# Kernel optimization log

Measured on AMD Instinct MI355X. Metric: run time of the kernel, lower is better.

Reference implementation:

```python
import jax, jax.numpy as jnp
import numpy as np

H = 8  # heads hardcoded in LightGFormer


def layernorm(x, g, b, eps=1e-5):
    m = x.mean(-1, keepdims=True)
    v = ((x - m) ** 2).mean(-1, keepdims=True)
    return (x - m) / jnp.sqrt(v + eps) * g + b


def setup_inputs() -> dict:
    key = jax.random.key(0)
    B, N, D, L = 16, 512, 256, 4
    Dff = 4 * D
    ks = jax.random.split(key, 12)

    def w(k, shape, scale=0.02):
        return jax.random.normal(k, shape, jnp.float32) * scale

    return {
        "input": w(ks[0], (B, N, D), 1.0),
        "input_v": w(ks[1], (B, N, D), 1.0),
        "pos_emb": w(ks[2], (N, D)),
        "Wq": w(ks[3], (L, D, D)), "bq": jnp.zeros((L, D), jnp.float32),
        "Wk": w(ks[4], (L, D, D)), "bk": jnp.zeros((L, D), jnp.float32),
        "Wv": w(ks[5], (L, D, D)), "bv": jnp.zeros((L, D), jnp.float32),
        "Wo": w(ks[6], (L, D, D)), "bo": jnp.zeros((L, D), jnp.float32),
        "W1": w(ks[7], (L, D, Dff)), "b1": jnp.zeros((L, Dff), jnp.float32),
        "W2": w(ks[8], (L, Dff // 2, D // 2)), "b2": jnp.zeros((L, D // 2), jnp.float32),
        "g1": jnp.ones((L, D), jnp.float32), "be1": jnp.zeros((L, D), jnp.float32),
        "g2": jnp.ones((L, D), jnp.float32), "be2": jnp.zeros((L, D), jnp.float32),
        "gf": jnp.ones((D,), jnp.float32), "bf": jnp.zeros((D,), jnp.float32),
        "mask": jax.random.randint(ks[9], (N, N), 0, 2) > 0,
    }


def reference(input, input_v, pos_emb, Wq, bq, Wk, bk, Wv, bv, Wo, bo,
              W1, b1, W2, b2, g1, be1, g2, be2, gf, bf, mask):
    B, N, D = input.shape
    L = Wq.shape[0]
    dk = D // H
    scale = 1.0 / float(np.sqrt(dk))

    x = input + pos_emb[None]       # learned positional encoding
    xv = input_v + pos_emb[None]    # values stream (never updated across layers)

    for i in range(L):
        # --- self-attention: queries/keys from x, values from xv ---
        q = (x @ Wq[i] + bq[i]).reshape(B, N, H, dk)
        k = (x @ Wk[i] + bk[i]).reshape(B, N, H, dk)
        v = (xv @ Wv[i] + bv[i]).reshape(B, N, H, dk)
        att = jnp.einsum('bqhd,bkhd->bhqk', q, k) * scale
        if i % 2 == 1:  # odd layers use the mask (Lightformer alternation)
            att = jnp.where(mask[None, None], -jnp.inf, att)
        att = jax.nn.softmax(att, axis=-1)
        o = jnp.einsum('bhqk,bkhd->bqhd', att, v).reshape(B, N, D)
        o = o @ Wo[i] + bo[i]
        x = layernorm(x + o, g1[i], be1[i])
        # --- FFN with grouped second linear: [.., 2, 2D] @ [2D, D/2] ---
        h = jax.nn.gelu(x @ W1[i] + b1[i], approximate=False)
        h = (h.reshape(B, N, 2, 2 * D) @ W2[i] + b2[i]).reshape(B, N, D)
        x = layernorm(x + h, g2[i], be2[i])

    x = layernorm(x, gf, bf)  # final attention_norm
    return x
```

## Files before the change

kernel.cpp:

```cpp
#include <hip/hip_runtime.h>
#include <hip/hip_bf16.h>
#include <math.h>

#define BDIM 16
#define NSEQ 512
#define DMODEL 256
#define NLAYER 4
#define NHEAD 8
#define DK 32
#define DFF 1024
#define BN (BDIM * NSEQ)
#define ND (NSEQ * DMODEL)

typedef __bf16 bf16x8 __attribute__((ext_vector_type(8)));
typedef float floatx4 __attribute__((ext_vector_type(4)));
typedef unsigned uint32x2 __attribute__((ext_vector_type(2)));

static __device__ __forceinline__ unsigned short f2bf(float f) {
    unsigned u = __float_as_uint(f);
    unsigned r = (u + 0x7FFFu + ((u >> 16) & 1u)) >> 16;
    return (unsigned short)r;
}

static __device__ __forceinline__ void async_ld16(const unsigned short* g,
                                                  unsigned short* l) {
    __builtin_amdgcn_global_load_lds(
        (const __attribute__((address_space(1))) unsigned int*)g,
        (__attribute__((address_space(3))) unsigned int*)l, 16, 0, 0);
}

static __device__ __forceinline__ float gelu_f(float c) {
    float u = 0.7978845608028654f * (c + 0.044715f * c * c * c);
    return c * (1.f / (1.f + __expf(-2.f * u)));
}

__global__ void conv_all_kernel(const float* __restrict__ Wq, const float* __restrict__ Wk,
                                const float* __restrict__ Wv, const float* __restrict__ Wo,
                                const float* __restrict__ W1, const float* __restrict__ W2,
                                const int* __restrict__ mask,
                                unsigned short* __restrict__ wqT, unsigned short* __restrict__ wkT,
                                unsigned short* __restrict__ wvT, unsigned short* __restrict__ woT,
                                unsigned short* __restrict__ w1T, unsigned short* __restrict__ w2T,
                                unsigned* __restrict__ bits) {
    int blk = blockIdx.x, tid = threadIdx.x;
    if (blk < 4096) {
        int i = blk * 256 + tid;
        int sel = i >> 18;
        int j = i & 262143;
        int l = j >> 16, rem = j & 65535, kk = rem >> 8, n = rem & 255;
        const float* src = sel == 0 ? Wq : sel == 1 ? Wk : sel == 2 ? Wv : Wo;
        unsigned short* dst = sel == 0 ? wqT : sel == 1 ? wkT : sel == 2 ? wvT : woT;
        dst[(size_t)l * 65536 + n * 256 + kk] = f2bf(src[j]);
    } else if (blk < 8192) {
        int i = (blk - 4096) * 256 + tid;
        int l = i >> 18, rem = i & 262143, kk = rem >> 10, n = rem & 1023;
        w1T[(size_t)l * 262144 + (size_t)n * 256 + kk] = f2bf(W1[i]);
    } else if (blk < 9216) {
        int j = (blk - 8192) * 256 + tid;
        int l = j >> 16, rem = j & 65535, kk = rem >> 7, n = rem & 127;
        w2T[(size_t)l * 65536 + (size_t)n * 512 + kk] = f2bf(W2[j]);
    } else {
        int w = (blk - 9216) * 256 + tid;
        int r = w >> 4, wi = w & 15;
        const int* src = mask + r * NSEQ + wi * 32;
        unsigned acc = 0;
#pragma unroll
        for (int j = 0; j < 32; j++) acc |= (src[j] != 0 ? 1u : 0u) << j;
        bits[w] = acc;
    }
}

__global__ void add_pos_kernel(const float* __restrict__ in,
                               const float* __restrict__ inv,
                               const float* __restrict__ pos,
                               float* __restrict__ x,
                               unsigned short* __restrict__ xb,
                               unsigned short* __restrict__ xvb,
                               int total) {
    int i = blockIdx.x * blockDim.x + threadIdx.x;
    if (i < total) {
        float pe = pos[i % ND];
        float a = in[i] + pe;
        float b = inv[i] + pe;
        x[i] = a;
        xb[i] = f2bf(a);
        xvb[i] = f2bf(b);
    }
}

__global__ __launch_bounds__(256) void qkv_mfma_kernel(
        const unsigned short* __restrict__ xb,
        const unsigned short* __restrict__ xvb,
        const unsigned short* __restrict__ WqT, const unsigned short* __restrict__ WkT,
        const unsigned short* __restrict__ WvT,
        const float* __restrict__ bq, const float* __restrict__ bk,
        const float* __restrict__ bv,
        unsigned short* __restrict__ qo, unsigned short* __restrict__ ko,
        unsigned short* __restrict__ vo) {
    int proj = blockIdx.x >> 1;
    const unsigned short* A  = (proj == 2) ? xvb : xb;
    const unsigned short* Bt = (proj == 0) ? WqT : (proj == 1) ? WkT : WvT;
    const float* bias        = (proj == 0) ? bq  : (proj == 1) ? bk  : bv;
    unsigned short* Cb       = (proj == 0) ? qo  : (proj == 1) ? ko  : vo;
    float qscale = (proj == 0) ? 0.17677669529663687f : 1.f;

    __shared__ unsigned short As[128 * 32];
    __shared__ unsigned short Bs[128 * 32];
    int tid = threadIdx.x;
    int wave = tid >> 6, lane = tid & 63;
    int rowBase = blockIdx.y * 128, colBase = (blockIdx.x & 1) * 128;
    int m0w = (wave & 1) * 64, n0w = (wave >> 1) * 64;
    int lr = lane & 15, quad = lane >> 4;
    int qx = quad ^ (lr & 3);

    floatx4 acc[4][4];
#pragma unroll
    for (int mi = 0; mi < 4; mi++)
#pragma unroll
        for (int nj = 0; nj < 4; nj++) acc[mi][nj] = (floatx4)0.0f;

    for (int kt = 0; kt < DMODEL; kt += 32) {
#pragma unroll
        for (int t = 0; t < 2; t++) {
            int idx = t * 256 + tid;
            int row = idx >> 2, kv8 = ((idx ^ row) & 3) * 8;
            async_ld16(A + (size_t)(rowBase + row) * DMODEL + kt + kv8, &As[idx * 8]);
            async_ld16(Bt + (size_t)(colBase + row) * DMODEL + kt + kv8, &Bs[idx * 8]);
        }
        __syncthreads();
        bf16x8 af[4], bfr[4];
#pragma unroll
        for (int mi = 0; mi < 4; mi++)
            af[mi] = *(const bf16x8*)&As[(m0w + mi * 16 + lr) * 32 + qx * 8];
#pragma unroll
        for (int nj = 0; nj < 4; nj++)
            bfr[nj] = *(const bf16x8*)&Bs[(n0w + nj * 16 + lr) * 32 + qx * 8];
#pragma unroll
        for (int mi = 0; mi < 4; mi++)
#pragma unroll
            for (int nj = 0; nj < 4; nj++)
                acc[mi][nj] = __builtin_amdgcn_mfma_f32_16x16x32_bf16(
                    af[mi], bfr[nj], acc[mi][nj], 0, 0, 0);
        __syncthreads();
    }

#pragma unroll
    for (int mi = 0; mi < 4; mi++) {
#pragma unroll
        for (int r = 0; r < 4; r++) {
            int grow = rowBase + m0w + mi * 16 + quad * 4 + r;
#pragma unroll
            for (int nj = 0; nj < 4; nj++) {
                int gcol = colBase + n0w + nj * 16 + lr;
                float c = (acc[mi][nj][r] + bias[gcol]) * qscale;
                size_t off = ((size_t)((grow >> 9) * 8 + (gcol >> 5)) << 14)
                           + (size_t)(grow & 511) * 32 + (gcol & 31);
                Cb[off] = f2bf(c);
            }
        }
    }
}

__global__ __launch_bounds__(256) void gemm_mfma_kernel(
        const unsigned short* __restrict__ A,
        const unsigned short* __restrict__ Bt,
        const float* __restrict__ bias,
        unsigned short* __restrict__ Cb,
        int M, int K, int N, int act) {
    __shared__ unsigned short As[128 * 32];
    __shared__ unsigned short Bs[128 * 32];
    int tid = threadIdx.x;
    int wave = tid >> 6, lane = tid & 63;
    int rowBase = blockIdx.y * 128, colBase = blockIdx.x * 128;
    int m0w = (wave & 1) * 64, n0w = (wave >> 1) * 64;
    int lr = lane & 15, quad = lane >> 4;
    int qx = quad ^ (lr & 3);

    floatx4 acc[4][4];
#pragma unroll
    for (int mi = 0; mi < 4; mi++)
#pragma unroll
        for (int nj = 0; nj < 4; nj++) acc[mi][nj] = (floatx4)0.0f;

    for (int kt = 0; kt < K; kt += 32) {
#pragma unroll
        for (int t = 0; t < 2; t++) {
            int idx = t * 256 + tid;
            int row = idx >> 2, kv8 = ((idx ^ row) & 3) * 8;
            async_ld16(A + (size_t)(rowBase + row) * K + kt + kv8, &As[idx * 8]);
            async_ld16(Bt + (size_t)(colBase + row) * K + kt + kv8, &Bs[idx * 8]);
        }
        __syncthreads();
        bf16x8 af[4], bfr[4];
#pragma unroll
        for (int mi = 0; mi < 4; mi++)
            af[mi] = *(const bf16x8*)&As[(m0w + mi * 16 + lr) * 32 + qx * 8];
#pragma unroll
        for (int nj = 0; nj < 4; nj++)
            bfr[nj] = *(const bf16x8*)&Bs[(n0w + nj * 16 + lr) * 32 + qx * 8];
#pragma unroll
        for (int mi = 0; mi < 4; mi++)
#pragma unroll
            for (int nj = 0; nj < 4; nj++)
                acc[mi][nj] = __builtin_amdgcn_mfma_f32_16x16x32_bf16(
                    af[mi], bfr[nj], acc[mi][nj], 0, 0, 0);
        __syncthreads();
    }

#pragma unroll
    for (int mi = 0; mi < 4; mi++) {
#pragma unroll
        for (int r = 0; r < 4; r++) {
            int grow = rowBase + m0w + mi * 16 + quad * 4 + r;
#pragma unroll
            for (int nj = 0; nj < 4; nj++) {
                int gcol = colBase + n0w + nj * 16 + lr;
                float c = acc[mi][nj][r] + bias[gcol];
                if (act) c = gelu_f(c);
                Cb[(size_t)grow * N + gcol] = f2bf(c);
            }
        }
    }
}

__global__ __launch_bounds__(64) void wo_ln_kernel(
        const unsigned short* __restrict__ A,
        const unsigned short* __restrict__ Bt,
        const float* __restrict__ bias,
        const float* __restrict__ g, const float* __restrict__ be,
        float* __restrict__ xf, unsigned short* __restrict__ xb) {
    __shared__ unsigned short As[16 * 32];
    __shared__ unsigned short Bs[256 * 32];
    int tid = threadIdx.x;
    int l16 = tid & 15, quad = tid >> 4;
    int rowBase = blockIdx.x * 16;
    int qx = quad ^ (l16 & 3);

    floatx4 acc[16];
#pragma unroll
    for (int t = 0; t < 16; t++) acc[t] = (floatx4)0.0f;

    for (int kt = 0; kt < 256; kt += 32) {
        {
            int row = tid >> 2, kv8 = ((tid ^ row) & 3) * 8;
            async_ld16(A + (size_t)(rowBase + row) * 256 + kt + kv8, &As[tid * 8]);
        }
#pragma unroll
        for (int t = 0; t < 16; t++) {
            int idx = t * 64 + tid;
            int row = idx >> 2, kv8 = ((idx ^ row) & 3) * 8;
            async_ld16(Bt + (size_t)row * 256 + kt + kv8, &Bs[idx * 8]);
        }
        __syncthreads();
        bf16x8 af = *(const bf16x8*)&As[l16 * 32 + qx * 8];
#pragma unroll
        for (int t = 0; t < 16; t++) {
            bf16x8 bfr = *(const bf16x8*)&Bs[(t * 16 + l16) * 32 + qx * 8];
            acc[t] = __builtin_amdgcn_mfma_f32_16x16x32_bf16(af, bfr, acc[t], 0, 0, 0);
        }
        __syncthreads();
    }

    float bcol[16], gc[16], bec[16];
#pragma unroll
    for (int t = 0; t < 16; t++) {
        int c = t * 16 + l16;
        bcol[t] = bias[c]; gc[t] = g[c]; bec[t] = be[c];
    }
#pragma unroll
    for (int r = 0; r < 4; r++) {
        int grow = rowBase + quad * 4 + r;
        float v[16], s = 0.f, s2 = 0.f;
#pragma unroll
        for (int t = 0; t < 16; t++) {
            int c = t * 16 + l16;
            float val = acc[t][r] + bcol[t] + xf[(size_t)grow * 256 + c];
            v[t] = val; s += val; s2 += val * val;
        }
#pragma unroll
        for (int off = 1; off <= 8; off <<= 1) {
            s += __shfl_xor(s, off);
            s2 += __shfl_xor(s2, off);
        }
        float mean = s * (1.f / 256.f);
        float var = s2 * (1.f / 256.f) - mean * mean;
        float rstd = rsqrtf(var + 1e-5f);
#pragma unroll
        for (int t = 0; t < 16; t++) {
            int c = t * 16 + l16;
            float o = (v[t] - mean) * rstd * gc[t] + bec[t];
            xf[(size_t)grow * 256 + c] = o;
            xb[(size_t)grow * 256 + c] = f2bf(o);
        }
    }
}

__global__ __launch_bounds__(128) void ffn2_ln_kernel(
        const unsigned short* __restrict__ A,
        const unsigned short* __restrict__ Bt,
        const float* __restrict__ bias,
        const float* __restrict__ g, const float* __restrict__ be,
        float* __restrict__ xf, unsigned short* __restrict__ xb) {
    __shared__ unsigned short As[64 * 32];
    __shared__ unsigned short Bs[128 * 32];
    __shared__ float redS[64][2], redQ[64][2];
    int tid = threadIdx.x;
    int wave = tid >> 6, lane = tid & 63, l16 = lane & 15, quad = lane >> 4;
    int rowBase = blockIdx.x * 64;
    int n0w = wave * 64;
    int qx = quad ^ (l16 & 3);

    floatx4 acc[4][4];
#pragma unroll
    for (int mi = 0; mi < 4; mi++)
#pragma unroll
        for (int nj = 0; nj < 4; nj++) acc[mi][nj] = (floatx4)0.0f;

    for (int kt = 0; kt < 512; kt += 32) {
#pragma unroll
        for (int t = 0; t < 2; t++) {
            int idx = t * 128 + tid;
            int row = idx >> 2, kv8 = ((idx ^ row) & 3) * 8;
            async_ld16(A + (size_t)(rowBase + row) * 512 + kt + kv8, &As[idx * 8]);
        }
#pragma unroll
        for (int t = 0; t < 4; t++) {
            int idx = t * 128 + tid;
            int row = idx >> 2, kv8 = ((idx ^ row) & 3) * 8;
            async_ld16(Bt + (size_t)row * 512 + kt + kv8, &Bs[idx * 8]);
        }
        __syncthreads();
        bf16x8 af[4], bfr[4];
#pragma unroll
        for (int mi = 0; mi < 4; mi++)
            af[mi] = *(const bf16x8*)&As[(mi * 16 + l16) * 32 + qx * 8];
#pragma unroll
        for (int nj = 0; nj < 4; nj++)
            bfr[nj] = *(const bf16x8*)&Bs[(n0w + nj * 16 + l16) * 32 + qx * 8];
#pragma unroll
        for (int mi = 0; mi < 4; mi++)
#pragma unroll
            for (int nj = 0; nj < 4; nj++)
                acc[mi][nj] = __builtin_amdgcn_mfma_f32_16x16x32_bf16(
                    af[mi], bfr[nj], acc[mi][nj], 0, 0, 0);
        __syncthreads();
    }

#pragma unroll
    for (int mi = 0; mi < 4; mi++) {
#pragma unroll
        for (int r = 0; r < 4; r++) {
            int row = mi * 16 + quad * 4 + r;
            int grow = rowBase + row;
            int token = grow >> 1, dbase = (grow & 1) * 128;
            float s = 0.f, s2 = 0.f;
#pragma unroll
            for (int nj = 0; nj < 4; nj++) {
                int gcol = n0w + nj * 16 + l16;
                float val = acc[mi][nj][r] + bias[gcol]
                          + xf[(size_t)token * 256 + dbase + gcol];
                acc[mi][nj][r] = val;
                s += val; s2 += val * val;
            }
#pragma unroll
            for (int off = 1; off <= 8; off <<= 1) {
                s += __shfl_xor(s, off);
                s2 += __shfl_xor(s2, off);
            }
            if (l16 == 0) { redS[row][wave] = s; redQ[row][wave] = s2; }
        }
    }
    __syncthreads();

#pragma unroll
    for (int mi = 0; mi < 4; mi++) {
#pragma unroll
        for (int r = 0; r < 4; r++) {
            int row = mi * 16 + quad * 4 + r;
            int grow = rowBase + row;
            int token = grow >> 1, dbase = (grow & 1) * 128;
            float ts = redS[row][0] + redS[row][1] + redS[row ^ 1][0] + redS[row ^ 1][1];
            float tq = redQ[row][0] + redQ[row][1] + redQ[row ^ 1][0] + redQ[row ^ 1][1];
            float mean = ts * (1.f / 256.f);
            float var = tq * (1.f / 256.f) - mean * mean;
            float rstd = rsqrtf(var + 1e-5f);
#pragma unroll
            for (int nj = 0; nj < 4; nj++) {
                int gcol = n0w + nj * 16 + l16;
                int d = dbase + gcol;
                float o = (acc[mi][nj][r] - mean) * rstd * g[d] + be[d];
                xf[(size_t)token * 256 + d] = o;
                xb[(size_t)token * 256 + d] = f2bf(o);
            }
        }
    }
}

__global__ __launch_bounds__(256, 4) void attn_mfma_kernel(
        const unsigned short* __restrict__ q, const unsigned short* __restrict__ k,
        const unsigned short* __restrict__ v, unsigned short* __restrict__ o,
        const unsigned* __restrict__ mbits_g, int use_mask) {
    int bid = blockIdx.x;
    int qg = bid >> 7;
    int bh = bid & 127;
    int h = bh & 7, b = bh >> 3;
    int tid = threadIdx.x;

    __shared__ unsigned short Vs[2][NSEQ * 16];

    const unsigned short* kbase = k + (size_t)(b * 8 + h) * (NSEQ * DK);
    const unsigned short* vbase = v + (size_t)(b * 8 + h) * (NSEQ * DK);

#pragma unroll
    for (int db = 0; db < 2; db++) {
#pragma unroll
        for (int t = 0; t < 4; t++) {
            int c = t * 256 + tid;
            int kk = c >> 1, half = c & 1;
            async_ld16(vbase + (size_t)kk * 32 + db * 16 + half * 8,
                       &Vs[db][c * 8]);
        }
    }

    int wave = tid >> 6, lane = tid & 63, l16 = lane & 15, quad = lane >> 4;
    int qbase = qg * 64 + wave * 16;

    bf16x8 qf = *(const bf16x8*)(q + ((size_t)(b * 8 + h) * NSEQ + qbase + l16) * 32 + quad * 8);

    unsigned mw[16];
    if (use_mask) {
        const uint4* mr = (const uint4*)(mbits_g + (size_t)(qbase + l16) * 16);
#pragma unroll
        for (int w = 0; w < 4; w++) *(uint4*)&mw[w * 4] = mr[w];
    } else {
#pragma unroll
        for (int w = 0; w < 16; w++) mw[w] = 0;
    }
    __syncthreads();

    unsigned va0 = (unsigned)(size_t)&Vs[0][0] + (unsigned)(lane * 8);
    unsigned va1 = (unsigned)(size_t)&Vs[1][0] + (unsigned)(lane * 8);

    const unsigned short* kfrag = kbase + (size_t)l16 * DK + quad * 8;

    floatx4 oT0 = (floatx4)0.f, oT1 = (floatx4)0.f;
    float m_run = -INFINITY, l_part = 0.f;

    uint32x2 t00, t01, t10, t11;
#define TR_ISSUE(cc)                                                      \
    asm volatile("ds_read_b64_tr_b16 %0, %4\n\t"                          \
                 "ds_read_b64_tr_b16 %1, %4 offset:512\n\t"               \
                 "ds_read_b64_tr_b16 %2, %5\n\t"                          \
                 "ds_read_b64_tr_b16 %3, %5 offset:512"                   \
                 : "=&v"(t00), "=&v"(t01), "=&v"(t10), "=&v"(t11)         \
                 : "v"(va0 + (unsigned)((cc) * 1024)),                    \
                   "v"(va1 + (unsigned)((cc) * 1024)))
    TR_ISSUE(0);

    bf16x8 k0 = *(const bf16x8*)(kfrag);
    bf16x8 k1 = *(const bf16x8*)(kfrag + 16 * DK);

#pragma unroll
    for (int c = 0; c < 16; c++) {
        floatx4 s0 = __builtin_amdgcn_mfma_f32_16x16x32_bf16(k0, qf, (floatx4)0.f, 0, 0, 0);
        floatx4 s1 = __builtin_amdgcn_mfma_f32_16x16x32_bf16(k1, qf, (floatx4)0.f, 0, 0, 0);

        bf16x8 k0n, k1n;
        if (c < 15) {
            k0n = *(const bf16x8*)(kfrag + (size_t)((c + 1) * 32) * DK);
            k1n = *(const bf16x8*)(kfrag + (size_t)((c + 1) * 32 + 16) * DK);
        }

        float sv[8];
#pragma unroll
        for (int r = 0; r < 4; r++) { sv[r] = s0[r]; sv[4 + r] = s1[r]; }
        if (use_mask) {
            unsigned wb = mw[c];
#pragma unroll
            for (int r = 0; r < 4; r++) {
                if ((wb >> (quad * 4 + r)) & 1) sv[r] = -INFINITY;
                if ((wb >> (16 + quad * 4 + r)) & 1) sv[4 + r] = -INFINITY;
            }
        }
        float mx = fmaxf(fmaxf(fmaxf(sv[0], sv[1]), fmaxf(sv[2], sv[3])),
                         fmaxf(fmaxf(sv[4], sv[5]), fmaxf(sv[6], sv[7])));
        mx = fmaxf(mx, __shfl_xor(mx, 16));
        mx = fmaxf(mx, __shfl_xor(mx, 32));
        if (!__all(mx <= m_run)) {
            float mnew = fmaxf(m_run, mx);
            float corr = (m_run == mnew) ? 1.f : __expf(m_run - mnew);
            l_part *= corr;
            oT0 *= corr; oT1 *= corr;
            m_run = mnew;
        }
        float p[8];
#pragma unroll
        for (int j = 0; j < 8; j++) {
            float e = __expf(sv[j] - m_run);
            p[j] = (sv[j] > -INFINITY) ? e : 0.f;
            l_part += p[j];
        }
        union { bf16x8 v8; unsigned u[4]; } pf;
#pragma unroll
        for (int j = 0; j < 4; j++)
            asm("v_cvt_pk_bf16_f32 %0, %1, %2"
                : "=v"(pf.u[j]) : "v"(p[2 * j]), "v"(p[2 * j + 1]));

        asm volatile("s_waitcnt lgkmcnt(0)");
        __builtin_amdgcn_sched_barrier(0);
        union { bf16x8 v8; uint32x2 u[2]; } av0, av1;
        av0.u[0] = t00; av0.u[1] = t01;
        av1.u[0] = t10; av1.u[1] = t11;

        oT0 = __builtin_amdgcn_mfma_f32_16x16x32_bf16(av0.v8, pf.v8, oT0, 0, 0, 0);
        oT1 = __builtin_amdgcn_mfma_f32_16x16x32_bf16(av1.v8, pf.v8, oT1, 0, 0, 0);
        if (c < 15) TR_ISSUE(c + 1);
        k0 = k0n; k1 = k1n;
    }
#undef TR_ISSUE

    float l = l_part;
    l += __shfl_xor(l, 16);
    l += __shfl_xor(l, 32);
    float invl = (l > 0.f) ? 1.f / l : 0.f;

    unsigned short* orow = o + ((size_t)(b * NSEQ + qbase + l16)) * DMODEL + h * DK;
#pragma unroll
    for (int r = 0; r < 4; r++) {
        orow[quad * 4 + r]      = f2bf(oT0[r] * invl);
        orow[16 + quad * 4 + r] = f2bf(oT1[r] * invl);
    }
}

__global__ __launch_bounds__(256) void final_ln_kernel(
        const float* __restrict__ a,
        const float* __restrict__ g, const float* __restrict__ be,
        float* __restrict__ out) {
    int t = blockIdx.x;
    int d = threadIdx.x;
    size_t idx = (size_t)t * DMODEL + d;
    float v = a[idx];
    float s = v, s2 = v * v;
#pragma unroll
    for (int off = 32; off; off >>= 1) {
        s  += __shfl_xor(s, off);
        s2 += __shfl_xor(s2, off);
    }
    __shared__ float ws1[4], ws2[4];
    int wid = d >> 6;
    if ((d & 63) == 0) { ws1[wid] = s; ws2[wid] = s2; }
    __syncthreads();
    s  = ws1[0] + ws1[1] + ws1[2] + ws1[3];
    s2 = ws2[0] + ws2[1] + ws2[2] + ws2[3];
    float mean = s * (1.f / DMODEL);
    float var = s2 * (1.f / DMODEL) - mean * mean;
    float rstd = rsqrtf(var + 1e-5f);
    out[idx] = (v - mean) * rstd * g[d] + be[d];
}

extern "C" void kernel_launch(void* const* d_in, const int* in_sizes, int n_in,
                              void* d_out, int out_size, void* d_ws, size_t ws_size,
                              hipStream_t stream) {
    const float* input  = (const float*)d_in[0];
    const float* inputv = (const float*)d_in[1];
    const float* pos    = (const float*)d_in[2];
    const float* Wq = (const float*)d_in[3];
    const float* bq = (const float*)d_in[4];
    const float* Wk = (const float*)d_in[5];
    const float* bk = (const float*)d_in[6];
    const float* Wv = (const float*)d_in[7];
    const float* bv = (const float*)d_in[8];
    const float* Wo = (const float*)d_in[9];
    const float* bo = (const float*)d_in[10];
    const float* W1 = (const float*)d_in[11];
    const float* b1 = (const float*)d_in[12];
    const float* W2 = (const float*)d_in[13];
    const float* b2 = (const float*)d_in[14];
    const float* g1 = (const float*)d_in[15];
    const float* be1 = (const float*)d_in[16];
    const float* g2 = (const float*)d_in[17];
    const float* be2 = (const float*)d_in[18];
    const float* gf = (const float*)d_in[19];
    const float* bff = (const float*)d_in[20];
    const int* mask = (const int*)d_in[21];

    float* out = (float*)d_out;

    char* wsb = (char*)d_ws;
    float* x_f  = (float*)(wsb + ((size_t)0 << 20));
    unsigned short* x_b  = (unsigned short*)(wsb + ((size_t)8 << 20));
    unsigned short* xv_b = (unsigned short*)(wsb + ((size_t)12 << 20));
    unsigned short* qb_b = (unsigned short*)(wsb + ((size_t)16 << 20));
    unsigned short* kb_b = (unsigned short*)(wsb + ((size_t)20 << 20));
    unsigned short* vb_b = (unsigned short*)(wsb + ((size_t)24 << 20));
    unsigned short* ab_b = (unsigned short*)(wsb + ((size_t)28 << 20));
    unsigned short* h_b  = qb_b;
    unsigned short* wqT = (unsigned short*)(wsb + ((size_t)32 << 20));
    unsigned short* wkT = wqT + (size_t)4 * 65536;
    unsigned short* wvT = wkT + (size_t)4 * 65536;
    unsigned short* woT = wvT + (size_t)4 * 65536;
    unsigned short* w1T = woT + (size_t)4 * 65536;
    unsigned short* w2T = w1T + (size_t)4 * 262144;
    unsigned* mbits = (unsigned*)(wsb + ((size_t)37 << 20));

    const size_t TOK = (size_t)BN * DMODEL;

    conv_all_kernel<<<9248, 256, 0, stream>>>(Wq, Wk, Wv, Wo, W1, W2, mask,
                                              wqT, wkT, wvT, woT, w1T, w2T, mbits);
    add_pos_kernel<<<(int)((TOK + 255) / 256), 256, 0, stream>>>(
        input, inputv, pos, x_f, x_b, xv_b, (int)TOK);

    for (int i = 0; i < NLAYER; i++) {
        const unsigned short* WqT_i = wqT + (size_t)i * 65536;
        const unsigned short* WkT_i = wkT + (size_t)i * 65536;
        const unsigned short* WvT_i = wvT + (size_t)i * 65536;
        const unsigned short* WoT_i = woT + (size_t)i * 65536;
        const unsigned short* W1T_i = w1T + (size_t)i * 262144;
        const unsigned short* W2T_i = w2T + (size_t)i * 65536;

        qkv_mfma_kernel<<<dim3(6, 64), 256, 0, stream>>>(
            x_b, xv_b, WqT_i, WkT_i, WvT_i,
            bq + i * DMODEL, bk + i * DMODEL, bv + i * DMODEL,
            qb_b, kb_b, vb_b);

        attn_mfma_kernel<<<BDIM * NHEAD * 8, 256, 0, stream>>>(
            qb_b, kb_b, vb_b, ab_b, mbits, (i & 1));

        wo_ln_kernel<<<BN / 16, 64, 0, stream>>>(
            ab_b, WoT_i, bo + i * DMODEL,
            g1 + i * DMODEL, be1 + i * DMODEL, x_f, x_b);

        gemm_mfma_kernel<<<dim3(8, 64), 256, 0, stream>>>(
            x_b, W1T_i, b1 + i * DFF, h_b, BN, DMODEL, DFF, 1);

        ffn2_ln_kernel<<<(2 * BN) / 64, 128, 0, stream>>>(
            h_b, W2T_i, b2 + i * (DMODEL / 2),
            g2 + i * DMODEL, be2 + i * DMODEL, x_f, x_b);
    }

    final_ln_kernel<<<BN, DMODEL, 0, stream>>>(x_f, gf, bff, out);
}
```

Before: 454.6 us.

## Fuse Wo+LN1, FFN1+GELU, FFN2+LN2 and final LN into one kernel per layer

Replaces the separate Wo+LayerNorm, W1 GEMM with GELU, W2+LayerNorm and final LayerNorm kernels with one fused per-16-token kernel. The intermediate activations (post-LN1 x and the GELU hidden) stay in LDS and are read with transposed LDS reads. Weights are pre-swizzled into MFMA fragment order so they can be loaded straight from global memory, and attention writes its output in fragment-panel layout. This removes the round trip of the large FFN hidden tensor through global memory and several launches. In exchange, each 16-row block re-reads every layer weight from global or cache, and parallelism per block is small.

```diff
diff --git a/kernel.cpp b/kernel.cpp
--- a/kernel.cpp
+++ b/kernel.cpp
@@ -21,6 +21,9 @@
     unsigned r = (u + 0x7FFFu + ((u >> 16) & 1u)) >> 16;
     return (unsigned short)r;
 }
+static __device__ __forceinline__ float bf2f(unsigned short u) {
+    return __uint_as_float(((unsigned)u) << 16);
+}
 
 static __device__ __forceinline__ void async_ld16(const unsigned short* g,
                                                   unsigned short* l) {
@@ -34,31 +37,54 @@
     return c * (1.f / (1.f + __expf(-2.f * u)));
 }
 
+static __device__ __forceinline__ unsigned cvtpk(float lo, float hi) {
+    unsigned r;
+    asm("v_cvt_pk_bf16_f32 %0, %1, %2" : "=v"(r) : "v"(lo), "v"(hi));
+    return r;
+}
+
 __global__ void conv_all_kernel(const float* __restrict__ Wq, const float* __restrict__ Wk,
                                 const float* __restrict__ Wv, const float* __restrict__ Wo,
                                 const float* __restrict__ W1, const float* __restrict__ W2,
                                 const int* __restrict__ mask,
                                 unsigned short* __restrict__ wqT, unsigned short* __restrict__ wkT,
-                                unsigned short* __restrict__ wvT, unsigned short* __restrict__ woT,
-                                unsigned short* __restrict__ w1T, unsigned short* __restrict__ w2T,
+                                unsigned short* __restrict__ wvT,
+                                unsigned short* __restrict__ wo_s,
+                                unsigned short* __restrict__ w1_s, unsigned short* __restrict__ w2_s,
                                 unsigned* __restrict__ bits) {
     int blk = blockIdx.x, tid = threadIdx.x;
-    if (blk < 4096) {
+    if (blk < 3072) {
         int i = blk * 256 + tid;
         int sel = i >> 18;
         int j = i & 262143;
         int l = j >> 16, rem = j & 65535, kk = rem >> 8, n = rem & 255;
-        const float* src = sel == 0 ? Wq : sel == 1 ? Wk : sel == 2 ? Wv : Wo;
-        unsigned short* dst = sel == 0 ? wqT : sel == 1 ? wkT : sel == 2 ? wvT : woT;
+        const float* src = sel == 0 ? Wq : sel == 1 ? Wk : Wv;
+        unsigned short* dst = sel == 0 ? wqT : sel == 1 ? wkT : wvT;
         dst[(size_t)l * 65536 + n * 256 + kk] = f2bf(src[j]);
+    } else if (blk < 4096) {
+        int i = (blk - 3072) * 256 + tid;
+        int l = i >> 16, o = i & 65535;
+        int j = o & 7, quad = (o >> 3) & 3, l16 = (o >> 5) & 15;
+        int kt = (o >> 9) & 7, cg = (o >> 12) & 15;
+        int k = kt * 32 + (j >> 2) * 16 + quad * 4 + (j & 3);
+        int dout = cg * 16 + l16;
+        wo_s[(size_t)l * 65536 + o] = f2bf(Wo[(size_t)l * 65536 + k * 256 + dout]);
     } else if (blk < 8192) {
         int i = (blk - 4096) * 256 + tid;
-        int l = i >> 18, rem = i & 262143, kk = rem >> 10, n = rem & 1023;
-        w1T[(size_t)l * 262144 + (size_t)n * 256 + kk] = f2bf(W1[i]);
+        int l = i >> 18, o = i & 262143;
+        int j = o & 7, quad = (o >> 3) & 3, l16 = (o >> 5) & 15;
+        int kt = (o >> 9) & 7, cg = (o >> 12) & 63;
+        int k = kt * 32 + (j >> 2) * 16 + quad * 4 + (j & 3);
+        int dout = cg * 16 + l16;
+        w1_s[(size_t)l * 262144 + o] = f2bf(W1[(size_t)l * 262144 + k * 1024 + dout]);
     } else if (blk < 9216) {
-        int j = (blk - 8192) * 256 + tid;
-        int l = j >> 16, rem = j & 65535, kk = rem >> 7, n = rem & 127;
-        w2T[(size_t)l * 65536 + (size_t)n * 512 + kk] = f2bf(W2[j]);
+        int i = (blk - 8192) * 256 + tid;
+        int l = i >> 16, o = i & 65535;
+        int j = o & 7, quad = (o >> 3) & 3, l16 = (o >> 5) & 15;
+        int kt = (o >> 9) & 15, cg = (o >> 13) & 7;
+        int k = kt * 32 + (j >> 2) * 16 + quad * 4 + (j & 3);
+        int dout = cg * 16 + l16;
+        w2_s[(size_t)l * 65536 + o] = f2bf(W2[(size_t)l * 65536 + k * 128 + dout]);
     } else {
         int w = (blk - 9216) * 256 + tid;
         int r = w >> 4, wi = w & 15;
@@ -161,244 +187,257 @@
     }
 }
 
-__global__ __launch_bounds__(256) void gemm_mfma_kernel(
-        const unsigned short* __restrict__ A,
-        const unsigned short* __restrict__ Bt,
-        const float* __restrict__ bias,
-        unsigned short* __restrict__ Cb,
-        int M, int K, int N, int act) {
-    __shared__ unsigned short As[128 * 32];
-    __shared__ unsigned short Bs[128 * 32];
+__global__ __launch_bounds__(256) void ffn_fused_kernel(
+        const unsigned short* __restrict__ ab_f,
+        const unsigned short* __restrict__ wo_s,
+        const unsigned short* __restrict__ w1_s,
+        const unsigned short* __restrict__ w2_s,
+        const float* __restrict__ bo,
+        const float* __restrict__ g1, const float* __restrict__ be1,
+        const float* __restrict__ b1,
+        const float* __restrict__ b2,
+        const float* __restrict__ g2, const float* __restrict__ be2,
+        const float* __restrict__ gf, const float* __restrict__ bf_,
+        float* __restrict__ xf, unsigned short* __restrict__ xb,
+        float* __restrict__ outF, int finalize) {
+    __shared__ unsigned short X1s[8 * 512];
+    __shared__ unsigned short Hs[16 * 512];
+    __shared__ float redA[16][4], redB[16][4];
+    __shared__ float redC[16][4], redD[16][4];
+    __shared__ float redE[16][4], redF[16][4];
+
     int tid = threadIdx.x;
-    int wave = tid >> 6, lane = tid & 63;
-    int rowBase = blockIdx.y * 128, colBase = blockIdx.x * 128;
-    int m0w = (wave & 1) * 64, n0w = (wave >> 1) * 64;
-    int lr = lane & 15, quad = lane >> 4;
-    int qx = quad ^ (lr & 3);
-
-    floatx4 acc[4][4];
-#pragma unroll
-    for (int mi = 0; mi < 4; mi++)
-#pragma unroll
-        for (int nj = 0; nj < 4; nj++) acc[mi][nj] = (floatx4)0.0f;
-
-    for (int kt = 0; kt < K; kt += 32) {
-#pragma unroll
-        for (int t = 0; t < 2; t++) {
-            int idx = t * 256 + tid;
-            int row = idx >> 2, kv8 = ((idx ^ row) & 3) * 8;
-            async_ld16(A + (size_t)(rowBase + row) * K + kt + kv8, &As[idx * 8]);
-            async_ld16(Bt + (size_t)(colBase + row) * K + kt + kv8, &Bs[idx * 8]);
-        }
-        __syncthreads();
-        bf16x8 af[4], bfr[4];
-#pragma unroll
-        for (int mi = 0; mi < 4; mi++)
-            af[mi] = *(const bf16x8*)&As[(m0w + mi * 16 + lr) * 32 + qx * 8];
-#pragma unroll
-        for (int nj = 0; nj < 4; nj++)
-            bfr[nj] = *(const bf16x8*)&Bs[(n0w + nj * 16 + lr) * 32 + qx * 8];
-#pragma unroll
-        for (int mi = 0; mi < 4; mi++)
-#pragma unroll
-            for (int nj = 0; nj < 4; nj++)
-                acc[mi][nj] = __builtin_amdgcn_mfma_f32_16x16x32_bf16(
-                    af[mi], bfr[nj], acc[mi][nj], 0, 0, 0);
-        __syncthreads();
-    }
-
-#pragma unroll
-    for (int mi = 0; mi < 4; mi++) {
-#pragma unroll
-        for (int r = 0; r < 4; r++) {
-            int grow = rowBase + m0w + mi * 16 + quad * 4 + r;
-#pragma unroll
-            for (int nj = 0; nj < 4; nj++) {
-                int gcol = colBase + n0w + nj * 16 + lr;
-                float c = acc[mi][nj][r] + bias[gcol];
-                if (act) c = gelu_f(c);
-                Cb[(size_t)grow * N + gcol] = f2bf(c);
-            }
-        }
-    }
-}
-
-__global__ __launch_bounds__(64) void wo_ln_kernel(
-        const unsigned short* __restrict__ A,
-        const unsigned short* __restrict__ Bt,
-        const float* __restrict__ bias,
-        const float* __restrict__ g, const float* __restrict__ be,
-        float* __restrict__ xf, unsigned short* __restrict__ xb) {
-    __shared__ unsigned short As[16 * 32];
-    __shared__ unsigned short Bs[256 * 32];
-    int tid = threadIdx.x;
-    int l16 = tid & 15, quad = tid >> 4;
-    int rowBase = blockIdx.x * 16;
-    int qx = quad ^ (l16 & 3);
-
-    floatx4 acc[16];
-#pragma unroll
-    for (int t = 0; t < 16; t++) acc[t] = (floatx4)0.0f;
-
-    for (int kt = 0; kt < 256; kt += 32) {
-        {
-            int row = tid >> 2, kv8 = ((tid ^ row) & 3) * 8;
-            async_ld16(A + (size_t)(rowBase + row) * 256 + kt + kv8, &As[tid * 8]);
-        }
-#pragma unroll
-        for (int t = 0; t < 16; t++) {
-            int idx = t * 64 + tid;
-            int row = idx >> 2, kv8 = ((idx ^ row) & 3) * 8;
-            async_ld16(Bt + (size_t)row * 256 + kt + kv8, &Bs[idx * 8]);
-        }
-        __syncthreads();
-        bf16x8 af = *(const bf16x8*)&As[l16 * 32 + qx * 8];
-#pragma unroll
-        for (int t = 0; t < 16; t++) {
-            bf16x8 bfr = *(const bf16x8*)&Bs[(t * 16 + l16) * 32 + qx * 8];
-            acc[t] = __builtin_amdgcn_mfma_f32_16x16x32_bf16(af, bfr, acc[t], 0, 0, 0);
-        }
-        __syncthreads();
-    }
-
-    float bcol[16], gc[16], bec[16];
-#pragma unroll
-    for (int t = 0; t < 16; t++) {
-        int c = t * 16 + l16;
-        bcol[t] = bias[c]; gc[t] = g[c]; bec[t] = be[c];
-    }
+    int w = tid >> 6, lane = tid & 63, l16 = lane & 15, quad = lane >> 4;
+    int bid = blockIdx.x;
+    int rowBase = bid * 16;
+    int fo = (l16 * 4 + quad) * 8;
+
+#define TR2(d0, d1, addr)                                                  \
+    asm volatile("ds_read_b64_tr_b16 %0, %2\n\t"                           \
+                 "ds_read_b64_tr_b16 %1, %2 offset:512"                    \
+                 : "=&v"(d0), "=&v"(d1) : "v"(addr))
+
+    floatx4 accA[4];
+#pragma unroll
+    for (int cg = 0; cg < 4; cg++) accA[cg] = (floatx4)0.0f;
+
+#pragma unroll
+    for (int kt = 0; kt < 8; kt++) {
+        bf16x8 af = *(const bf16x8*)(ab_f + ((size_t)bid * 8 + kt) * 512 + fo);
+        bf16x8 bfr[4];
+#pragma unroll
+        for (int cg = 0; cg < 4; cg++)
+            bfr[cg] = *(const bf16x8*)(wo_s + ((size_t)((w * 4 + cg) * 8 + kt)) * 512 + fo);
+#pragma unroll
+        for (int cg = 0; cg < 4; cg++)
+            accA[cg] = __builtin_amdgcn_mfma_f32_16x16x32_bf16(af, bfr[cg], accA[cg], 0, 0, 0);
+    }
+
 #pragma unroll
     for (int r = 0; r < 4; r++) {
-        int grow = rowBase + quad * 4 + r;
-        float v[16], s = 0.f, s2 = 0.f;
-#pragma unroll
-        for (int t = 0; t < 16; t++) {
-            int c = t * 16 + l16;
-            float val = acc[t][r] + bcol[t] + xf[(size_t)grow * 256 + c];
-            v[t] = val; s += val; s2 += val * val;
+        int tok = quad * 4 + r;
+        float s = 0.f, s2 = 0.f;
+#pragma unroll
+        for (int cg = 0; cg < 4; cg++) {
+            int col = w * 64 + cg * 16 + l16;
+            float v = accA[cg][r] + bo[col] + xf[(size_t)(rowBase + tok) * 256 + col];
+            accA[cg][r] = v; s += v; s2 += v * v;
         }
 #pragma unroll
         for (int off = 1; off <= 8; off <<= 1) {
             s += __shfl_xor(s, off);
             s2 += __shfl_xor(s2, off);
         }
-        float mean = s * (1.f / 256.f);
-        float var = s2 * (1.f / 256.f) - mean * mean;
+        if (l16 == 0) { redA[tok][w] = s; redB[tok][w] = s2; }
+    }
+    __syncthreads();
+#pragma unroll
+    for (int r = 0; r < 4; r++) {
+        int tok = quad * 4 + r;
+        float ts = redA[tok][0] + redA[tok][1] + redA[tok][2] + redA[tok][3];
+        float tq = redB[tok][0] + redB[tok][1] + redB[tok][2] + redB[tok][3];
+        float mean = ts * (1.f / 256.f);
+        float var = tq * (1.f / 256.f) - mean * mean;
         float rstd = rsqrtf(var + 1e-5f);
 #pragma unroll
-        for (int t = 0; t < 16; t++) {
-            int c = t * 16 + l16;
-            float o = (v[t] - mean) * rstd * gc[t] + bec[t];
-            xf[(size_t)grow * 256 + c] = o;
-            xb[(size_t)grow * 256 + c] = f2bf(o);
-        }
-    }
-}
-
-__global__ __launch_bounds__(128) void ffn2_ln_kernel(
-        const unsigned short* __restrict__ A,
-        const unsigned short* __restrict__ Bt,
-        const float* __restrict__ bias,
-        const float* __restrict__ g, const float* __restrict__ be,
-        float* __restrict__ xf, unsigned short* __restrict__ xb) {
-    __shared__ unsigned short As[64 * 32];
-    __shared__ unsigned short Bs[128 * 32];
-    __shared__ float redS[64][2], redQ[64][2];
-    int tid = threadIdx.x;
-    int wave = tid >> 6, lane = tid & 63, l16 = lane & 15, quad = lane >> 4;
-    int rowBase = blockIdx.x * 64;
-    int n0w = wave * 64;
-    int qx = quad ^ (l16 & 3);
-
-    floatx4 acc[4][4];
-#pragma unroll
-    for (int mi = 0; mi < 4; mi++)
-#pragma unroll
-        for (int nj = 0; nj < 4; nj++) acc[mi][nj] = (floatx4)0.0f;
-
-    for (int kt = 0; kt < 512; kt += 32) {
-#pragma unroll
-        for (int t = 0; t < 2; t++) {
-            int idx = t * 128 + tid;
-            int row = idx >> 2, kv8 = ((idx ^ row) & 3) * 8;
-            async_ld16(A + (size_t)(rowBase + row) * 512 + kt + kv8, &As[idx * 8]);
-        }
-#pragma unroll
-        for (int t = 0; t < 4; t++) {
-            int idx = t * 128 + tid;
-            int row = idx >> 2, kv8 = ((idx ^ row) & 3) * 8;
-            async_ld16(Bt + (size_t)row * 512 + kt + kv8, &Bs[idx * 8]);
+        for (int cg = 0; cg < 4; cg++) {
+            int col = w * 64 + cg * 16 + l16;
+            accA[cg][r] = (accA[cg][r] - mean) * rstd * g1[col] + be1[col];
+        }
+    }
+#pragma unroll
+    for (int cg = 0; cg < 4; cg++) {
+        int col = w * 64 + cg * 16 + l16;
+        int ct = col >> 5, colL = col & 31;
+        uint32x2 pk;
+        pk[0] = cvtpk(accA[cg][0], accA[cg][1]);
+        pk[1] = cvtpk(accA[cg][2], accA[cg][3]);
+        *(uint32x2*)&X1s[ct * 512 + colL * 16 + quad * 4] = pk;
+    }
+    __syncthreads();
+
+    unsigned x1addr = (unsigned)(size_t)&X1s[0] + (unsigned)(lane * 8);
+    unsigned haddr  = (unsigned)(size_t)&Hs[0]  + (unsigned)(lane * 8);
+
+    floatx4 y[2][2];
+#pragma unroll
+    for (int g = 0; g < 2; g++)
+#pragma unroll
+        for (int cj = 0; cj < 2; cj++) y[g][cj] = (floatx4)0.0f;
+
+    for (int g = 0; g < 2; g++) {
+        floatx4 accB[8];
+#pragma unroll
+        for (int c = 0; c < 8; c++) accB[c] = (floatx4)0.0f;
+
+        uint32x2 ta, tb;
+        TR2(ta, tb, x1addr);
+#pragma unroll
+        for (int kt = 0; kt < 8; kt++) {
+            bf16x8 bfr[8];
+#pragma unroll
+            for (int c = 0; c < 8; c++)
+                bfr[c] = *(const bf16x8*)(w1_s +
+                    ((size_t)((g * 32 + w * 8 + c) * 8 + kt)) * 512 + fo);
+            asm volatile("s_waitcnt lgkmcnt(0)");
+            __builtin_amdgcn_sched_barrier(0);
+            union { bf16x8 v8; uint32x2 u[2]; } afu;
+            afu.u[0] = ta; afu.u[1] = tb;
+            bf16x8 af = afu.v8;
+            if (kt < 7) TR2(ta, tb, x1addr + (unsigned)((kt + 1) * 1024));
+#pragma unroll
+            for (int c = 0; c < 8; c++)
+                accB[c] = __builtin_amdgcn_mfma_f32_16x16x32_bf16(af, bfr[c], accB[c], 0, 0, 0);
+        }
+#pragma unroll
+        for (int c = 0; c < 8; c++) {
+            int col = w * 128 + c * 16 + l16;
+            float bb = b1[g * 512 + col];
+            float o0 = gelu_f(accB[c][0] + bb);
+            float o1 = gelu_f(accB[c][1] + bb);
+            float o2 = gelu_f(accB[c][2] + bb);
+            float o3 = gelu_f(accB[c][3] + bb);
+            int ct = col >> 5, colL = col & 31;
+            uint32x2 pk;
+            pk[0] = cvtpk(o0, o1);
+            pk[1] = cvtpk(o2, o3);
+            *(uint32x2*)&Hs[ct * 512 + colL * 16 + quad * 4] = pk;
         }
         __syncthreads();
-        bf16x8 af[4], bfr[4];
-#pragma unroll
-        for (int mi = 0; mi < 4; mi++)
-            af[mi] = *(const bf16x8*)&As[(mi * 16 + l16) * 32 + qx * 8];
-#pragma unroll
-        for (int nj = 0; nj < 4; nj++)
-            bfr[nj] = *(const bf16x8*)&Bs[(n0w + nj * 16 + l16) * 32 + qx * 8];
-#pragma unroll
-        for (int mi = 0; mi < 4; mi++)
-#pragma unroll
-            for (int nj = 0; nj < 4; nj++)
-                acc[mi][nj] = __builtin_amdgcn_mfma_f32_16x16x32_bf16(
-                    af[mi], bfr[nj], acc[mi][nj], 0, 0, 0);
-        __syncthreads();
-    }
-
-#pragma unroll
-    for (int mi = 0; mi < 4; mi++) {
+
+        TR2(ta, tb, haddr);
+#pragma unroll
+        for (int kt = 0; kt < 16; kt++) {
+            bf16x8 bfr[2];
+#pragma unroll
+            for (int cj = 0; cj < 2; cj++)
+                bfr[cj] = *(const bf16x8*)(w2_s +
+                    ((size_t)((w * 2 + cj) * 16 + kt)) * 512 + fo);
+            asm volatile("s_waitcnt lgkmcnt(0)");
+            __builtin_amdgcn_sched_barrier(0);
+            union { bf16x8 v8; uint32x2 u[2]; } afu;
+            afu.u[0] = ta; afu.u[1] = tb;
+            bf16x8 af = afu.v8;
+            if (kt < 15) TR2(ta, tb, haddr + (unsigned)((kt + 1) * 1024));
+#pragma unroll
+            for (int cj = 0; cj < 2; cj++)
+                y[g][cj] = __builtin_amdgcn_mfma_f32_16x16x32_bf16(af, bfr[cj], y[g][cj], 0, 0, 0);
+        }
+        if (g == 0) __syncthreads();
+    }
+#undef TR2
+
+#pragma unroll
+    for (int r = 0; r < 4; r++) {
+        int tok = quad * 4 + r;
+        float s = 0.f, s2 = 0.f;
+#pragma unroll
+        for (int g = 0; g < 2; g++)
+#pragma unroll
+            for (int cj = 0; cj < 2; cj++) {
+                int cc = (w * 2 + cj) * 16 + l16;
+                int col = g * 128 + cc;
+                float x1v = bf2f(X1s[(col >> 5) * 512 + (col & 31) * 16 + tok]);
+                float v = y[g][cj][r] + b2[cc] + x1v;
+                y[g][cj][r] = v; s += v; s2 += v * v;
+            }
+#pragma unroll
+        for (int off = 1; off <= 8; off <<= 1) {
+            s += __shfl_xor(s, off);
+            s2 += __shfl_xor(s2, off);
+        }
+        if (l16 == 0) { redC[tok][w] = s; redD[tok][w] = s2; }
+    }
+    __syncthreads();
+
+    if (!finalize) {
 #pragma unroll
         for (int r = 0; r < 4; r++) {
-            int row = mi * 16 + quad * 4 + r;
-            int grow = rowBase + row;
-            int token = grow >> 1, dbase = (grow & 1) * 128;
-            float s = 0.f, s2 = 0.f;
-#pragma unroll
-            for (int nj = 0; nj < 4; nj++) {
-                int gcol = n0w + nj * 16 + l16;
-                float val = acc[mi][nj][r] + bias[gcol]
-                          + xf[(size_t)token * 256 + dbase + gcol];
-                acc[mi][nj][r] = val;
-                s += val; s2 += val * val;
-            }
-#pragma unroll
-            for (int off = 1; off <= 8; off <<= 1) {
-                s += __shfl_xor(s, off);
-                s2 += __shfl_xor(s2, off);
-            }
-            if (l16 == 0) { redS[row][wave] = s; redQ[row][wave] = s2; }
-        }
-    }
-    __syncthreads();
-
-#pragma unroll
-    for (int mi = 0; mi < 4; mi++) {
-#pragma unroll
-        for (int r = 0; r < 4; r++) {
-            int row = mi * 16 + quad * 4 + r;
-            int grow = rowBase + row;
-            int token = grow >> 1, dbase = (grow & 1) * 128;
-            float ts = redS[row][0] + redS[row][1] + redS[row ^ 1][0] + redS[row ^ 1][1];
-            float tq = redQ[row][0] + redQ[row][1] + redQ[row ^ 1][0] + redQ[row ^ 1][1];
+            int tok = quad * 4 + r;
+            float ts = redC[tok][0] + redC[tok][1] + redC[tok][2] + redC[tok][3];
+            float tq = redD[tok][0] + redD[tok][1] + redD[tok][2] + redD[tok][3];
             float mean = ts * (1.f / 256.f);
             float var = tq * (1.f / 256.f) - mean * mean;
             float rstd = rsqrtf(var + 1e-5f);
 #pragma unroll
-            for (int nj = 0; nj < 4; nj++) {
-                int gcol = n0w + nj * 16 + l16;
-                int d = dbase + gcol;
-                float o = (acc[mi][nj][r] - mean) * rstd * g[d] + be[d];
-                xf[(size_t)token * 256 + d] = o;
-                xb[(size_t)token * 256 + d] = f2bf(o);
+            for (int g = 0; g < 2; g++)
+#pragma unroll
+                for (int cj = 0; cj < 2; cj++) {
+                    int col = g * 128 + (w * 2 + cj) * 16 + l16;
+                    float o = (y[g][cj][r] - mean) * rstd * g2[col] + be2[col];
+                    xf[(size_t)(rowBase + tok) * 256 + col] = o;
+                    xb[(size_t)(rowBase + tok) * 256 + col] = f2bf(o);
+                }
+        }
+    } else {
+#pragma unroll
+        for (int r = 0; r < 4; r++) {
+            int tok = quad * 4 + r;
+            float ts = redC[tok][0] + redC[tok][1] + redC[tok][2] + redC[tok][3];
+            float tq = redD[tok][0] + redD[tok][1] + redD[tok][2] + redD[tok][3];
+            float mean = ts * (1.f / 256.f);
+            float var = tq * (1.f / 256.f) - mean * mean;
+            float rstd = rsqrtf(var + 1e-5f);
+            float s3 = 0.f, q3 = 0.f;
+#pragma unroll
+            for (int g = 0; g < 2; g++)
+#pragma unroll
+                for (int cj = 0; cj < 2; cj++) {
+                    int col = g * 128 + (w * 2 + cj) * 16 + l16;
+                    float o = (y[g][cj][r] - mean) * rstd * g2[col] + be2[col];
+                    y[g][cj][r] = o; s3 += o; q3 += o * o;
+                }
+#pragma unroll
+            for (int off = 1; off <= 8; off <<= 1) {
+                s3 += __shfl_xor(s3, off);
+                q3 += __shfl_xor(q3, off);
             }
+            if (l16 == 0) { redE[tok][w] = s3; redF[tok][w] = q3; }
+        }
+        __syncthreads();
+#pragma unroll
+        for (int r = 0; r < 4; r++) {
+            int tok = quad * 4 + r;
+            float ts = redE[tok][0] + redE[tok][1] + redE[tok][2] + redE[tok][3];
+            float tq = redF[tok][0] + redF[tok][1] + redF[tok][2] + redF[tok][3];
+            float mean = ts * (1.f / 256.f);
+            float var = tq * (1.f / 256.f) - mean * mean;
+            float rstd = rsqrtf(var + 1e-5f);
+#pragma unroll
+            for (int g = 0; g < 2; g++)
+#pragma unroll
+                for (int cj = 0; cj < 2; cj++) {
+                    int col = g * 128 + (w * 2 + cj) * 16 + l16;
+                    outF[(size_t)(rowBase + tok) * 256 + col]
+                        = (y[g][cj][r] - mean) * rstd * gf[col] + bf_[col];
+                }
         }
     }
 }
 
 __global__ __launch_bounds__(256, 4) void attn_mfma_kernel(
         const unsigned short* __restrict__ q, const unsigned short* __restrict__ k,
-        const unsigned short* __restrict__ v, unsigned short* __restrict__ o,
+        const unsigned short* __restrict__ v, unsigned short* __restrict__ ab_f,
         const unsigned* __restrict__ mbits_g, int use_mask) {
     int bid = blockIdx.x;
     int qg = bid >> 7;
@@ -503,8 +542,7 @@
         union { bf16x8 v8; unsigned u[4]; } pf;
 #pragma unroll
         for (int j = 0; j < 4; j++)
-            asm("v_cvt_pk_bf16_f32 %0, %1, %2"
-                : "=v"(pf.u[j]) : "v"(p[2 * j]), "v"(p[2 * j + 1]));
+            pf.u[j] = cvtpk(p[2 * j], p[2 * j + 1]);
 
         asm volatile("s_waitcnt lgkmcnt(0)");
         __builtin_amdgcn_sched_barrier(0);
@@ -524,38 +562,13 @@
     l += __shfl_xor(l, 32);
     float invl = (l > 0.f) ? 1.f / l : 0.f;
 
-    unsigned short* orow = o + ((size_t)(b * NSEQ + qbase + l16)) * DMODEL + h * DK;
-#pragma unroll
-    for (int r = 0; r < 4; r++) {
-        orow[quad * 4 + r]      = f2bf(oT0[r] * invl);
-        orow[16 + quad * 4 + r] = f2bf(oT1[r] * invl);
-    }
-}
-
-__global__ __launch_bounds__(256) void final_ln_kernel(
-        const float* __restrict__ a,
-        const float* __restrict__ g, const float* __restrict__ be,
-        float* __restrict__ out) {
-    int t = blockIdx.x;
-    int d = threadIdx.x;
-    size_t idx = (size_t)t * DMODEL + d;
-    float v = a[idx];
-    float s = v, s2 = v * v;
-#pragma unroll
-    for (int off = 32; off; off >>= 1) {
-        s  += __shfl_xor(s, off);
-        s2 += __shfl_xor(s2, off);
-    }
-    __shared__ float ws1[4], ws2[4];
-    int wid = d >> 6;
-    if ((d & 63) == 0) { ws1[wid] = s; ws2[wid] = s2; }
-    __syncthreads();
-    s  = ws1[0] + ws1[1] + ws1[2] + ws1[3];
-    s2 = ws2[0] + ws2[1] + ws2[2] + ws2[3];
-    float mean = s * (1.f / DMODEL);
-    float var = s2 * (1.f / DMODEL) - mean * mean;
-    float rstd = rsqrtf(var + 1e-5f);
-    out[idx] = (v - mean) * rstd * g[d] + be[d];
+    uint4 val;
+    val.x = cvtpk(oT0[0] * invl, oT0[1] * invl);
+    val.y = cvtpk(oT0[2] * invl, oT0[3] * invl);
+    val.z = cvtpk(oT1[0] * invl, oT1[1] * invl);
+    val.w = cvtpk(oT1[2] * invl, oT1[3] * invl);
+    size_t panel = (size_t)b * 32 + qg * 4 + wave;
+    *(uint4*)(ab_f + (panel * 8 + h) * 512 + (l16 * 4 + quad) * 8) = val;
 }
 
 extern "C" void kernel_launch(void* const* d_in, const int* in_sizes, int n_in,
@@ -593,20 +606,19 @@
     unsigned short* qb_b = (unsigned short*)(wsb + ((size_t)16 << 20));
     unsigned short* kb_b = (unsigned short*)(wsb + ((size_t)20 << 20));
     unsigned short* vb_b = (unsigned short*)(wsb + ((size_t)24 << 20));
-    unsigned short* ab_b = (unsigned short*)(wsb + ((size_t)28 << 20));
-    unsigned short* h_b  = qb_b;
+    unsigned short* ab_f = (unsigned short*)(wsb + ((size_t)28 << 20));
     unsigned short* wqT = (unsigned short*)(wsb + ((size_t)32 << 20));
     unsigned short* wkT = wqT + (size_t)4 * 65536;
     unsigned short* wvT = wkT + (size_t)4 * 65536;
-    unsigned short* woT = wvT + (size_t)4 * 65536;
-    unsigned short* w1T = woT + (size_t)4 * 65536;
-    unsigned short* w2T = w1T + (size_t)4 * 262144;
+    unsigned short* wo_s = wvT + (size_t)4 * 65536;
+    unsigned short* w1_s = wo_s + (size_t)4 * 65536;
+    unsigned short* w2_s = w1_s + (size_t)4 * 262144;
     unsigned* mbits = (unsigned*)(wsb + ((size_t)37 << 20));
 
     const size_t TOK = (size_t)BN * DMODEL;
 
     conv_all_kernel<<<9248, 256, 0, stream>>>(Wq, Wk, Wv, Wo, W1, W2, mask,
-                                              wqT, wkT, wvT, woT, w1T, w2T, mbits);
+                                              wqT, wkT, wvT, wo_s, w1_s, w2_s, mbits);
     add_pos_kernel<<<(int)((TOK + 255) / 256), 256, 0, stream>>>(
         input, inputv, pos, x_f, x_b, xv_b, (int)TOK);
 
@@ -614,9 +626,9 @@
         const unsigned short* WqT_i = wqT + (size_t)i * 65536;
         const unsigned short* WkT_i = wkT + (size_t)i * 65536;
         const unsigned short* WvT_i = wvT + (size_t)i * 65536;
-        const unsigned short* WoT_i = woT + (size_t)i * 65536;
-        const unsigned short* W1T_i = w1T + (size_t)i * 262144;
-        const unsigned short* W2T_i = w2T + (size_t)i * 65536;
+        const unsigned short* Wo_i  = wo_s + (size_t)i * 65536;
+        const unsigned short* W1_i  = w1_s + (size_t)i * 262144;
+        const unsigned short* W2_i  = w2_s + (size_t)i * 65536;
 
         qkv_mfma_kernel<<<dim3(6, 64), 256, 0, stream>>>(
             x_b, xv_b, WqT_i, WkT_i, WvT_i,
@@ -624,19 +636,13 @@
             qb_b, kb_b, vb_b);
 
         attn_mfma_kernel<<<BDIM * NHEAD * 8, 256, 0, stream>>>(
-            qb_b, kb_b, vb_b, ab_b, mbits, (i & 1));
-
-        wo_ln_kernel<<<BN / 16, 64, 0, stream>>>(
-            ab_b, WoT_i, bo + i * DMODEL,
-            g1 + i * DMODEL, be1 + i * DMODEL, x_f, x_b);
-
-        gemm_mfma_kernel<<<dim3(8, 64), 256, 0, stream>>>(
-            x_b, W1T_i, b1 + i * DFF, h_b, BN, DMODEL, DFF, 1);
-
-        ffn2_ln_kernel<<<(2 * BN) / 64, 128, 0, stream>>>(
-            h_b, W2T_i, b2 + i * (DMODEL / 2),
-            g2 + i * DMODEL, be2 + i * DMODEL, x_f, x_b);
-    }
-
-    final_ln_kernel<<<BN, DMODEL, 0, stream>>>(x_f, gf, bff, out);
-}
+            qb_b, kb_b, vb_b, ab_f, mbits, (i & 1));
+
+        ffn_fused_kernel<<<BN / 16, 256, 0, stream>>>(
+            ab_f, Wo_i, W1_i, W2_i,
+            bo + i * DMODEL, g1 + i * DMODEL, be1 + i * DMODEL,
+            b1 + i * DFF, b2 + i * (DMODEL / 2),
+            g2 + i * DMODEL, be2 + i * DMODEL,
+            gf, bff, x_f, x_b, out, (i == NLAYER - 1) ? 1 : 0);
+    }
+}
```

Result: faster. 418.7 us (-7.9%).
